# Kernel tuning notes

Measured on AMD Instinct MI355X. Metric: run time of the kernel, lower is better.

## Reference

```python
import jax, jax.numpy as jnp
import numpy as np

D_MODEL = 1024
D_HEAD = 64
N_HEADS = D_MODEL // D_HEAD
MAX_SEQ = 2048
BATCH = 2
SEQ = 2048


def setup_inputs() -> dict:
    key = jax.random.key(0)
    ks = jax.random.split(key, 10)
    s = 1.0 / np.sqrt(D_MODEL)
    return {
        "x": jax.random.normal(ks[0], (BATCH, SEQ, D_MODEL), dtype=jnp.float32),
        "Wq": jax.random.normal(ks[1], (D_MODEL, D_MODEL), dtype=jnp.float32) * s,
        "bq": jax.random.normal(ks[2], (D_MODEL,), dtype=jnp.float32) * 0.01,
        "Wk": jax.random.normal(ks[3], (D_MODEL, D_MODEL), dtype=jnp.float32) * s,
        "bk": jax.random.normal(ks[4], (D_MODEL,), dtype=jnp.float32) * 0.01,
        "Wv": jax.random.normal(ks[5], (D_MODEL, D_MODEL), dtype=jnp.float32) * s,
        "bv": jax.random.normal(ks[6], (D_MODEL,), dtype=jnp.float32) * 0.01,
        "Er": jax.random.normal(ks[7], (MAX_SEQ, D_HEAD), dtype=jnp.float32),
        "Wo": jax.random.normal(ks[8], (D_MODEL, D_MODEL), dtype=jnp.float32) * s,
        "bo": jax.random.normal(ks[9], (D_MODEL,), dtype=jnp.float32) * 0.01,
    }


def _s_rel(q, Er):
    # q: [B,H,S,Dh]; use last S rows of Er (start = max_seq - seq)
    S = q.shape[2]
    Er_slice = Er[Er.shape[0] - S:, :]                  # [S, Dh]
    qE = jnp.einsum("bhsd,ld->bhsl", q, Er_slice)       # [B,H,S,S]
    padded = jnp.pad(qE, ((0, 0), (0, 0), (0, 0), (1, 0)))  # [B,H,S,S+1]
    B, H, S1, S2 = padded.shape
    padded = padded.reshape(B, H, S2, S1)               # skew trick
    return padded[:, :, 1:, :]                          # [B,H,S,S]


def reference(x, Wq, bq, Wk, bk, Wv, bv, Er, Wo, bo):
    B, S, _ = x.shape
    scale = 1.0 / np.sqrt(D_HEAD)
    # projections (torch Linear: x @ W.T + b)
    def proj(W, b):
        return (x @ W.T + b).reshape(B, S, N_HEADS, D_HEAD).transpose(0, 2, 1, 3)
    q = proj(Wq, bq)   # [B,H,S,Dh]
    k = proj(Wk, bk)
    v = proj(Wv, bv)
    qk = jnp.einsum("bhsd,bhtd->bhst", q, k)            # [B,H,S,S]
    logits = (qk + _s_rel(q, Er)) * scale
    causal = jnp.tril(jnp.ones((S, S), dtype=bool))
    masked = jnp.where(causal[None, None], logits, -1e9)
    attn = jax.nn.softmax(masked, axis=-1)
    out = jnp.einsum("bhst,bhtd->bhsd", attn, v)        # [B,H,S,Dh]
    out = out.transpose(0, 2, 1, 3).reshape(B, S, D_MODEL)
    return out @ Wo.T + bo
```

## Files before the change

kernel.cpp:

```cpp
#include <hip/hip_runtime.h>
#include <hip/hip_bf16.h>

typedef short v8s __attribute__((ext_vector_type(8)));
typedef float v4f __attribute__((ext_vector_type(4)));
typedef __hip_bfloat16 bf16;

#define MFMA(a, b, c) __builtin_amdgcn_mfma_f32_16x16x32_bf16(a, b, c, 0, 0, 0)

__global__ __launch_bounds__(256) void cast_all(
    const float* __restrict__ x,  const float* __restrict__ wq,
    const float* __restrict__ wk, const float* __restrict__ wv,
    const float* __restrict__ wo, const float* __restrict__ er,
    bf16* __restrict__ xb,  bf16* __restrict__ wqb, bf16* __restrict__ wkb,
    bf16* __restrict__ wvb, bf16* __restrict__ wob, bf16* __restrict__ erb)
{
    const int r = blockIdx.y;
    const float* s; bf16* d; int n4;
    if      (r == 0) { s = x;  d = xb;  n4 = 1048576; }
    else if (r == 1) { s = wq; d = wqb; n4 = 262144;  }
    else if (r == 2) { s = wk; d = wkb; n4 = 262144;  }
    else if (r == 3) { s = wv; d = wvb; n4 = 262144;  }
    else if (r == 4) { s = wo; d = wob; n4 = 262144;  }
    else             { s = er; d = erb; n4 = 32768;   }
    const int i = blockIdx.x * 256 + threadIdx.x;
    if (i < n4) {
        const float4 v = ((const float4*)s)[i];
        bf16 t[4];
        t[0] = __float2bfloat16(v.x);
        t[1] = __float2bfloat16(v.y);
        t[2] = __float2bfloat16(v.z);
        t[3] = __float2bfloat16(v.w);
        ((uint2*)d)[i] = *(const uint2*)t;
    }
}

__global__ __launch_bounds__(256) void gemm_nt(
    const bf16* __restrict__ A,
    const bf16* __restrict__ W0, const bf16* __restrict__ W1, const bf16* __restrict__ W2,
    const float* __restrict__ b0, const float* __restrict__ b1, const float* __restrict__ b2,
    bf16* __restrict__ o0, bf16* __restrict__ o1, bf16* __restrict__ o2,
    float* __restrict__ outf, int headmajor)
{
    const int z = blockIdx.z;
    const bf16* W     = (z == 0) ? W0 : (z == 1) ? W1 : W2;
    const float* bias = (z == 0) ? b0 : (z == 1) ? b1 : b2;
    bf16* out         = (z == 0) ? o0 : (z == 1) ? o1 : o2;

    __shared__ bf16 As[128 * 40];
    __shared__ bf16 Bs[128 * 40];

    const int tid = threadIdx.x;
    const int w  = tid >> 6, l = tid & 63;
    const int lm = l & 15,  lq = l >> 4;
    const int wm = (w >> 1) * 64, wn = (w & 1) * 64;
    const int m0 = blockIdx.y * 128, n0 = blockIdx.x * 128;

    v4f acc[4][4];
#pragma unroll
    for (int i = 0; i < 4; ++i)
#pragma unroll
        for (int j = 0; j < 4; ++j) acc[i][j] = (v4f){0.f, 0.f, 0.f, 0.f};

    const int r0 = tid >> 2;
    const int c8 = (tid & 3) * 8;

    for (int k0 = 0; k0 < 1024; k0 += 32) {
        __syncthreads();
#pragma unroll
        for (int rep = 0; rep < 2; ++rep) {
            const int row = r0 + rep * 64;
            *(uint4*)&As[row * 40 + c8] = *(const uint4*)&A[(size_t)(m0 + row) * 1024 + k0 + c8];
            *(uint4*)&Bs[row * 40 + c8] = *(const uint4*)&W[(size_t)(n0 + row) * 1024 + k0 + c8];
        }
        __syncthreads();
        v8s a[4], b[4];
#pragma unroll
        for (int i = 0; i < 4; ++i) a[i] = *(const v8s*)&As[(wm + i * 16 + lm) * 40 + lq * 8];
#pragma unroll
        for (int j = 0; j < 4; ++j) b[j] = *(const v8s*)&Bs[(wn + j * 16 + lm) * 40 + lq * 8];
#pragma unroll
        for (int i = 0; i < 4; ++i)
#pragma unroll
            for (int j = 0; j < 4; ++j)
                acc[i][j] = MFMA(a[i], b[j], acc[i][j]);
    }

    float bv[4];
#pragma unroll
    for (int j = 0; j < 4; ++j) bv[j] = bias[n0 + wn + j * 16 + lm];

#pragma unroll
    for (int i = 0; i < 4; ++i) {
#pragma unroll
        for (int j = 0; j < 4; ++j) {
            const int col = n0 + wn + j * 16 + lm;
#pragma unroll
            for (int r = 0; r < 4; ++r) {
                const int row = m0 + wm + i * 16 + lq * 4 + r;
                const float v = acc[i][j][r] + bv[j];
                if (headmajor) {
                    const int bb = row >> 11, ss = row & 2047;
                    const int hh = col >> 6,  dd = col & 63;
                    out[((size_t)(bb * 16 + hh) * 2048 + ss) * 64 + dd] = __float2bfloat16(v);
                } else {
                    outf[(size_t)row * 1024 + col] = v;
                }
            }
        }
    }
}

__global__ __launch_bounds__(256) void vtrans(const bf16* __restrict__ V, bf16* __restrict__ Vt)
{
    __shared__ bf16 T[64 * 72];
    const int s0  = blockIdx.x * 64;
    const int bh  = blockIdx.y;
    const int tid = threadIdx.x;
#pragma unroll
    for (int rep = 0; rep < 2; ++rep) {
        const int unit = tid + rep * 256;
        const int sl = unit >> 3, d8 = (unit & 7) * 8;
        *(uint4*)&T[sl * 72 + d8] = *(const uint4*)&V[((size_t)bh * 2048 + s0 + sl) * 64 + d8];
    }
    __syncthreads();
#pragma unroll
    for (int rep = 0; rep < 2; ++rep) {
        const int unit = tid + rep * 256;
        const int d = unit >> 3, t8 = (unit & 7) * 8;
        unsigned short tmp[8];
#pragma unroll
        for (int j = 0; j < 8; ++j) tmp[j] = *(const unsigned short*)&T[(t8 + j) * 72 + d];
        *(uint4*)&Vt[((size_t)bh * 64 + d) * 2048 + s0 + t8] = *(const uint4*)tmp;
    }
}

__global__ __launch_bounds__(256, 4) void attn(
    const bf16* __restrict__ Q, const bf16* __restrict__ K,
    const bf16* __restrict__ Vt, const bf16* __restrict__ Er,
    bf16* __restrict__ AO)
{
    __shared__ bf16 Ks[64 * 72];
    __shared__ bf16 Vs[64 * 72];
    __shared__ bf16 Ps[64 * 72];
    __shared__ bf16 Gs[64 * 84];

    const int ord = blockIdx.x;
    const int u = ord & 255, j = ord >> 8;
    const int a = u & 31, yh = u >> 5;
    const int q1 = (j & 2) ? (a ^ 16) : a;
    const int qb = (j & 1) ? (31 - q1) : q1;
    const int bh = 8 * j + yh;

    const int i0 = qb * 64;
    const int b  = bh >> 4, h = bh & 15;
    const int tid = threadIdx.x;
    const int w  = tid >> 6, l = tid & 63;
    const int lm = l & 15,  lq = l >> 4;

    const bf16* qp = Q + ((size_t)bh * 2048 + i0 + w * 16 + lm) * 64 + lq * 8;
    const v8s q0 = *(const v8s*)qp;
    const v8s q1f = *(const v8s*)(qp + 32);

    v4f accO[4];
#pragma unroll
    for (int dt = 0; dt < 4; ++dt) accO[dt] = (v4f){0.f, 0.f, 0.f, 0.f};
    float rs[4];
#pragma unroll
    for (int r = 0; r < 4; ++r) rs[r] = 0.f;

    const int sr0 = tid >> 3;
    const int sc8 = (tid & 7) * 8;
    const size_t kbase = (size_t)bh * 2048 * 64;
    const size_t vbase = (size_t)bh * 64 * 2048;

    const int nk = qb + 1;

    uint4 kp0 = *(const uint4*)&K[kbase + (size_t)sr0 * 64 + sc8];
    uint4 kp1 = *(const uint4*)&K[kbase + (size_t)(sr0 + 32) * 64 + sc8];
    uint4 vp0 = *(const uint4*)&Vt[vbase + (size_t)sr0 * 2048 + sc8];
    uint4 vp1 = *(const uint4*)&Vt[vbase + (size_t)(sr0 + 32) * 2048 + sc8];

    for (int it = 0; it < nk; ++it) {
        const int j0 = it * 64;
        __syncthreads();
        *(uint4*)&Ks[sr0 * 72 + sc8]        = kp0;
        *(uint4*)&Ks[(sr0 + 32) * 72 + sc8] = kp1;
        *(uint4*)&Vs[sr0 * 72 + sc8]        = vp0;
        *(uint4*)&Vs[(sr0 + 32) * 72 + sc8] = vp1;
        if (it + 1 < nk) {
            const int jn = j0 + 64;
            kp0 = *(const uint4*)&K[kbase + (size_t)(jn + sr0) * 64 + sc8];
            kp1 = *(const uint4*)&K[kbase + (size_t)(jn + sr0 + 32) * 64 + sc8];
            vp0 = *(const uint4*)&Vt[vbase + (size_t)sr0 * 2048 + jn + sc8];
            vp1 = *(const uint4*)&Vt[vbase + (size_t)(sr0 + 32) * 2048 + jn + sc8];
        }
        const int basew = 2048 - 16 - i0 + j0 - 16 * w;
#pragma unroll
        for (int ct2 = 0; ct2 < 5; ++ct2) {
            int mr = basew + ct2 * 16 + lm;
            mr = (mr > 2047) ? 2047 : mr;
            const bf16* ep = Er + (size_t)mr * 64 + lq * 8;
            const v8s e0 = *(const v8s*)ep;
            const v8s e1 = *(const v8s*)(ep + 32);
            v4f g = (v4f){0.f, 0.f, 0.f, 0.f};
            g = MFMA(q0, e0, g);
            g = MFMA(q1f, e1, g);
#pragma unroll
            for (int r = 0; r < 4; ++r)
                Gs[(w * 16 + lq * 4 + r) * 84 + ct2 * 16 + lm] =
                    __float2bfloat16(g[r] * 0.125f);
        }
        __syncthreads();
        v4f sv[4];
#pragma unroll
        for (int ct = 0; ct < 4; ++ct) {
            const v8s k0f = *(const v8s*)&Ks[(ct * 16 + lm) * 72 + lq * 8];
            const v8s k1f = *(const v8s*)&Ks[(ct * 16 + lm) * 72 + 32 + lq * 8];
            v4f s = (v4f){0.f, 0.f, 0.f, 0.f};
            s = MFMA(q0, k0f, s);
            s = MFMA(q1f, k1f, s);
            sv[ct] = s;
        }
#pragma unroll
        for (int r = 0; r < 4; ++r) {
            const int rl = lq * 4 + r;
            const int ig = i0 + w * 16 + rl;
#pragma unroll
            for (int ct = 0; ct < 4; ++ct) {
                const int jj = ct * 16 + lm;
                const float gb = (float)Gs[(w * 16 + rl) * 84 + jj + 15 - rl];
                float s = fmaf(sv[ct][r], 0.125f, gb);
                if (j0 + jj > ig) s = -1e9f;
                const float pe = __expf(s - 4.0f);
                rs[r] += pe;
                Ps[(w * 16 + rl) * 72 + jj] = __float2bfloat16(pe);
            }
        }
        const v8s pa0 = *(const v8s*)&Ps[(w * 16 + lm) * 72 + lq * 8];
        const v8s pa1 = *(const v8s*)&Ps[(w * 16 + lm) * 72 + 32 + lq * 8];
#pragma unroll
        for (int dt = 0; dt < 4; ++dt) {
            const v8s vb0 = *(const v8s*)&Vs[(dt * 16 + lm) * 72 + lq * 8];
            const v8s vb1 = *(const v8s*)&Vs[(dt * 16 + lm) * 72 + 32 + lq * 8];
            accO[dt] = MFMA(pa0, vb0, accO[dt]);
            accO[dt] = MFMA(pa1, vb1, accO[dt]);
        }
    }
#pragma unroll
    for (int r = 0; r < 4; ++r) {
#pragma unroll
        for (int msk = 8; msk >= 1; msk >>= 1)
            rs[r] += __shfl_xor(rs[r], msk, 64);
    }
#pragma unroll
    for (int dt = 0; dt < 4; ++dt) {
#pragma unroll
        for (int r = 0; r < 4; ++r) {
            const int row = i0 + w * 16 + lq * 4 + r;
            const int d   = dt * 16 + lm;
            const float v = accO[dt][r] / rs[r];
            AO[((size_t)b * 2048 + row) * 1024 + h * 64 + d] = __float2bfloat16(v);
        }
    }
}

extern "C" void kernel_launch(void* const* d_in, const int* in_sizes, int n_in,
                              void* d_out, int out_size, void* d_ws, size_t ws_size,
                              hipStream_t stream)
{
    const float* x  = (const float*)d_in[0];
    const float* Wq = (const float*)d_in[1];
    const float* bq = (const float*)d_in[2];
    const float* Wk = (const float*)d_in[3];
    const float* bk = (const float*)d_in[4];
    const float* Wv = (const float*)d_in[5];
    const float* bv = (const float*)d_in[6];
    const float* Er = (const float*)d_in[7];
    const float* Wo = (const float*)d_in[8];
    const float* bo = (const float*)d_in[9];
    float* out = (float*)d_out;

    bf16* ws = (bf16*)d_ws;
    const size_t NEl = (size_t)4096 * 1024;
    bf16* Qw  = ws;
    bf16* Kw  = ws + NEl;
    bf16* Vw  = ws + 2 * NEl;
    bf16* Vtw = ws + 3 * NEl;
    bf16* xb  = ws + 4 * NEl;
    bf16* AOw = xb;
    bf16* Wqb = ws + 5 * NEl;
    bf16* Wkb = Wqb + 1024 * 1024;
    bf16* Wvb = Wkb + 1024 * 1024;
    bf16* Wob = Wvb + 1024 * 1024;
    bf16* Erb = Wob + 1024 * 1024;

    cast_all<<<dim3(4096, 6), 256, 0, stream>>>(x, Wq, Wk, Wv, Wo, Er,
                                                xb, Wqb, Wkb, Wvb, Wob, Erb);
    gemm_nt<<<dim3(8, 32, 3), 256, 0, stream>>>(xb, Wqb, Wkb, Wvb, bq, bk, bv,
                                                Qw, Kw, Vw, nullptr, 1);
    vtrans<<<dim3(32, 32), 256, 0, stream>>>(Vw, Vtw);
    attn<<<dim3(1024), 256, 0, stream>>>(Qw, Kw, Vtw, Erb, AOw);
    gemm_nt<<<dim3(8, 32, 1), 256, 0, stream>>>(AOw, Wob, Wob, Wob, bo, bo, bo,
                                                AOw, AOw, AOw, out, 0);
}
```

Measured before the change: 280.4 us.

## Split causal attention KV range across blocks with atomic partial sums

Attention work for long query blocks is split into up to four KV segments (2560 blocks instead of 1024). Each segment atomically adds its unnormalized output and row-sum into fp32 num/den buffers. The output projection GEMM normalizes and casts these on load, and the QKV GEMM casts x from fp32 on load, so the separate x cast disappears. This balances per-block work and raises parallelism, at the cost of a memset, fp32 atomics, and a larger fp32 intermediate read by the final GEMM. The fixed exp(s-4) shift with no running max is unchanged, so combining partial sums stays exact.

After: 297.4 us. 6.0% more time.

```diff
diff --git a/kernel.cpp b/kernel.cpp
--- a/kernel.cpp
+++ b/kernel.cpp
@@ -7,21 +7,20 @@
 
 #define MFMA(a, b, c) __builtin_amdgcn_mfma_f32_16x16x32_bf16(a, b, c, 0, 0, 0)
 
-__global__ __launch_bounds__(256) void cast_all(
-    const float* __restrict__ x,  const float* __restrict__ wq,
-    const float* __restrict__ wk, const float* __restrict__ wv,
-    const float* __restrict__ wo, const float* __restrict__ er,
-    bf16* __restrict__ xb,  bf16* __restrict__ wqb, bf16* __restrict__ wkb,
-    bf16* __restrict__ wvb, bf16* __restrict__ wob, bf16* __restrict__ erb)
+__global__ __launch_bounds__(256) void cast_w(
+    const float* __restrict__ wq, const float* __restrict__ wk,
+    const float* __restrict__ wv, const float* __restrict__ wo,
+    const float* __restrict__ er,
+    bf16* __restrict__ wqb, bf16* __restrict__ wkb, bf16* __restrict__ wvb,
+    bf16* __restrict__ wob, bf16* __restrict__ erb)
 {
     const int r = blockIdx.y;
     const float* s; bf16* d; int n4;
-    if      (r == 0) { s = x;  d = xb;  n4 = 1048576; }
-    else if (r == 1) { s = wq; d = wqb; n4 = 262144;  }
-    else if (r == 2) { s = wk; d = wkb; n4 = 262144;  }
-    else if (r == 3) { s = wv; d = wvb; n4 = 262144;  }
-    else if (r == 4) { s = wo; d = wob; n4 = 262144;  }
-    else             { s = er; d = erb; n4 = 32768;   }
+    if      (r == 0) { s = wq; d = wqb; n4 = 262144; }
+    else if (r == 1) { s = wk; d = wkb; n4 = 262144; }
+    else if (r == 2) { s = wv; d = wvb; n4 = 262144; }
+    else if (r == 3) { s = wo; d = wob; n4 = 262144; }
+    else             { s = er; d = erb; n4 = 32768;  }
     const int i = blockIdx.x * 256 + threadIdx.x;
     if (i < n4) {
         const float4 v = ((const float4*)s)[i];
@@ -34,12 +33,14 @@
     }
 }
 
+template<int MODE>
 __global__ __launch_bounds__(256) void gemm_nt(
-    const bf16* __restrict__ A,
+    const float* __restrict__ Af,
+    const float* __restrict__ num, const float* __restrict__ den,
     const bf16* __restrict__ W0, const bf16* __restrict__ W1, const bf16* __restrict__ W2,
     const float* __restrict__ b0, const float* __restrict__ b1, const float* __restrict__ b2,
     bf16* __restrict__ o0, bf16* __restrict__ o1, bf16* __restrict__ o2,
-    float* __restrict__ outf, int headmajor)
+    float* __restrict__ outf)
 {
     const int z = blockIdx.z;
     const bf16* W     = (z == 0) ? W0 : (z == 1) ? W1 : W2;
@@ -69,7 +70,29 @@
 #pragma unroll
         for (int rep = 0; rep < 2; ++rep) {
             const int row = r0 + rep * 64;
-            *(uint4*)&As[row * 40 + c8] = *(const uint4*)&A[(size_t)(m0 + row) * 1024 + k0 + c8];
+            bf16 t[8];
+            if (MODE == 0) {
+                const float4 f0 = *(const float4*)&Af[(size_t)(m0 + row) * 1024 + k0 + c8];
+                const float4 f1 = *(const float4*)&Af[(size_t)(m0 + row) * 1024 + k0 + c8 + 4];
+                t[0] = __float2bfloat16(f0.x); t[1] = __float2bfloat16(f0.y);
+                t[2] = __float2bfloat16(f0.z); t[3] = __float2bfloat16(f0.w);
+                t[4] = __float2bfloat16(f1.x); t[5] = __float2bfloat16(f1.y);
+                t[6] = __float2bfloat16(f1.z); t[7] = __float2bfloat16(f1.w);
+            } else {
+                const int rowg = m0 + row;
+                const int bb = rowg >> 11, ss = rowg & 2047;
+                const int col0 = k0 + c8;
+                const int hh = col0 >> 6, dd = col0 & 63;
+                const size_t rbase = ((size_t)(bb * 16 + hh) * 2048 + ss);
+                const float4 f0 = *(const float4*)&num[rbase * 64 + dd];
+                const float4 f1 = *(const float4*)&num[rbase * 64 + dd + 4];
+                const float rdn = 1.0f / den[rbase];
+                t[0] = __float2bfloat16(f0.x * rdn); t[1] = __float2bfloat16(f0.y * rdn);
+                t[2] = __float2bfloat16(f0.z * rdn); t[3] = __float2bfloat16(f0.w * rdn);
+                t[4] = __float2bfloat16(f1.x * rdn); t[5] = __float2bfloat16(f1.y * rdn);
+                t[6] = __float2bfloat16(f1.z * rdn); t[7] = __float2bfloat16(f1.w * rdn);
+            }
+            *(uint4*)&As[row * 40 + c8] = *(const uint4*)t;
             *(uint4*)&Bs[row * 40 + c8] = *(const uint4*)&W[(size_t)(n0 + row) * 1024 + k0 + c8];
         }
         __syncthreads();
@@ -98,7 +121,7 @@
             for (int r = 0; r < 4; ++r) {
                 const int row = m0 + wm + i * 16 + lq * 4 + r;
                 const float v = acc[i][j][r] + bv[j];
-                if (headmajor) {
+                if (MODE == 0) {
                     const int bb = row >> 11, ss = row & 2047;
                     const int hh = col >> 6,  dd = col & 63;
                     out[((size_t)(bb * 16 + hh) * 2048 + ss) * 64 + dd] = __float2bfloat16(v);
@@ -137,7 +160,7 @@
 __global__ __launch_bounds__(256, 4) void attn(
     const bf16* __restrict__ Q, const bf16* __restrict__ K,
     const bf16* __restrict__ Vt, const bf16* __restrict__ Er,
-    bf16* __restrict__ AO)
+    float* __restrict__ num, float* __restrict__ den)
 {
     __shared__ bf16 Ks[64 * 72];
     __shared__ bf16 Vs[64 * 72];
@@ -145,14 +168,18 @@
     __shared__ bf16 Gs[64 * 84];
 
     const int ord = blockIdx.x;
-    const int u = ord & 255, j = ord >> 8;
-    const int a = u & 31, yh = u >> 5;
-    const int q1 = (j & 2) ? (a ^ 16) : a;
-    const int qb = (j & 1) ? (31 - q1) : q1;
-    const int bh = 8 * j + yh;
+    const int bh  = ord / 80;
+    const int c   = 79 - (ord - bh * 80);
+    int qb, sp, ns;
+    if      (c < 8)  { qb = c;                  sp = 0;            ns = 1; }
+    else if (c < 24) { qb = 8  + ((c - 8) >> 1);  sp = (c - 8) & 1;  ns = 2; }
+    else if (c < 48) { qb = 16 + (c - 24) / 3;    sp = (c - 24) % 3; ns = 3; }
+    else             { qb = 24 + ((c - 48) >> 2); sp = (c - 48) & 3; ns = 4; }
+    const int n  = qb + 1;
+    const int t0 = (sp * n) / ns;
+    const int t1 = ((sp + 1) * n) / ns;
 
     const int i0 = qb * 64;
-    const int b  = bh >> 4, h = bh & 15;
     const int tid = threadIdx.x;
     const int w  = tid >> 6, l = tid & 63;
     const int lm = l & 15,  lq = l >> 4;
@@ -173,77 +200,78 @@
     const size_t kbase = (size_t)bh * 2048 * 64;
     const size_t vbase = (size_t)bh * 64 * 2048;
 
-    const int nk = qb + 1;
-
-    uint4 kp0 = *(const uint4*)&K[kbase + (size_t)sr0 * 64 + sc8];
-    uint4 kp1 = *(const uint4*)&K[kbase + (size_t)(sr0 + 32) * 64 + sc8];
-    uint4 vp0 = *(const uint4*)&Vt[vbase + (size_t)sr0 * 2048 + sc8];
-    uint4 vp1 = *(const uint4*)&Vt[vbase + (size_t)(sr0 + 32) * 2048 + sc8];
-
-    for (int it = 0; it < nk; ++it) {
-        const int j0 = it * 64;
-        __syncthreads();
-        *(uint4*)&Ks[sr0 * 72 + sc8]        = kp0;
-        *(uint4*)&Ks[(sr0 + 32) * 72 + sc8] = kp1;
-        *(uint4*)&Vs[sr0 * 72 + sc8]        = vp0;
-        *(uint4*)&Vs[(sr0 + 32) * 72 + sc8] = vp1;
-        if (it + 1 < nk) {
-            const int jn = j0 + 64;
-            kp0 = *(const uint4*)&K[kbase + (size_t)(jn + sr0) * 64 + sc8];
-            kp1 = *(const uint4*)&K[kbase + (size_t)(jn + sr0 + 32) * 64 + sc8];
-            vp0 = *(const uint4*)&Vt[vbase + (size_t)sr0 * 2048 + jn + sc8];
-            vp1 = *(const uint4*)&Vt[vbase + (size_t)(sr0 + 32) * 2048 + jn + sc8];
-        }
-        const int basew = 2048 - 16 - i0 + j0 - 16 * w;
-#pragma unroll
-        for (int ct2 = 0; ct2 < 5; ++ct2) {
-            int mr = basew + ct2 * 16 + lm;
-            mr = (mr > 2047) ? 2047 : mr;
-            const bf16* ep = Er + (size_t)mr * 64 + lq * 8;
-            const v8s e0 = *(const v8s*)ep;
-            const v8s e1 = *(const v8s*)(ep + 32);
-            v4f g = (v4f){0.f, 0.f, 0.f, 0.f};
-            g = MFMA(q0, e0, g);
-            g = MFMA(q1f, e1, g);
-#pragma unroll
-            for (int r = 0; r < 4; ++r)
-                Gs[(w * 16 + lq * 4 + r) * 84 + ct2 * 16 + lm] =
-                    __float2bfloat16(g[r] * 0.125f);
-        }
-        __syncthreads();
-        v4f sv[4];
-#pragma unroll
-        for (int ct = 0; ct < 4; ++ct) {
-            const v8s k0f = *(const v8s*)&Ks[(ct * 16 + lm) * 72 + lq * 8];
-            const v8s k1f = *(const v8s*)&Ks[(ct * 16 + lm) * 72 + 32 + lq * 8];
-            v4f s = (v4f){0.f, 0.f, 0.f, 0.f};
-            s = MFMA(q0, k0f, s);
-            s = MFMA(q1f, k1f, s);
-            sv[ct] = s;
-        }
-#pragma unroll
-        for (int r = 0; r < 4; ++r) {
-            const int rl = lq * 4 + r;
-            const int ig = i0 + w * 16 + rl;
+    {
+        const int j0 = t0 * 64;
+        uint4 kp0 = *(const uint4*)&K[kbase + (size_t)(j0 + sr0) * 64 + sc8];
+        uint4 kp1 = *(const uint4*)&K[kbase + (size_t)(j0 + sr0 + 32) * 64 + sc8];
+        uint4 vp0 = *(const uint4*)&Vt[vbase + (size_t)sr0 * 2048 + j0 + sc8];
+        uint4 vp1 = *(const uint4*)&Vt[vbase + (size_t)(sr0 + 32) * 2048 + j0 + sc8];
+
+        for (int it = t0; it < t1; ++it) {
+            const int j0i = it * 64;
+            __syncthreads();
+            *(uint4*)&Ks[sr0 * 72 + sc8]        = kp0;
+            *(uint4*)&Ks[(sr0 + 32) * 72 + sc8] = kp1;
+            *(uint4*)&Vs[sr0 * 72 + sc8]        = vp0;
+            *(uint4*)&Vs[(sr0 + 32) * 72 + sc8] = vp1;
+            if (it + 1 < t1) {
+                const int jn = j0i + 64;
+                kp0 = *(const uint4*)&K[kbase + (size_t)(jn + sr0) * 64 + sc8];
+                kp1 = *(const uint4*)&K[kbase + (size_t)(jn + sr0 + 32) * 64 + sc8];
+                vp0 = *(const uint4*)&Vt[vbase + (size_t)sr0 * 2048 + jn + sc8];
+                vp1 = *(const uint4*)&Vt[vbase + (size_t)(sr0 + 32) * 2048 + jn + sc8];
+            }
+            const int basew = 2048 - 16 - i0 + j0i - 16 * w;
+#pragma unroll
+            for (int ct2 = 0; ct2 < 5; ++ct2) {
+                int mr = basew + ct2 * 16 + lm;
+                mr = (mr > 2047) ? 2047 : mr;
+                const bf16* ep = Er + (size_t)mr * 64 + lq * 8;
+                const v8s e0 = *(const v8s*)ep;
+                const v8s e1 = *(const v8s*)(ep + 32);
+                v4f g = (v4f){0.f, 0.f, 0.f, 0.f};
+                g = MFMA(q0, e0, g);
+                g = MFMA(q1f, e1, g);
+#pragma unroll
+                for (int r = 0; r < 4; ++r)
+                    Gs[(w * 16 + lq * 4 + r) * 84 + ct2 * 16 + lm] =
+                        __float2bfloat16(g[r] * 0.125f);
+            }
+            __syncthreads();
+            v4f sv[4];
 #pragma unroll
             for (int ct = 0; ct < 4; ++ct) {
-                const int jj = ct * 16 + lm;
-                const float gb = (float)Gs[(w * 16 + rl) * 84 + jj + 15 - rl];
-                float s = fmaf(sv[ct][r], 0.125f, gb);
-                if (j0 + jj > ig) s = -1e9f;
-                const float pe = __expf(s - 4.0f);
-                rs[r] += pe;
-                Ps[(w * 16 + rl) * 72 + jj] = __float2bfloat16(pe);
-            }
-        }
-        const v8s pa0 = *(const v8s*)&Ps[(w * 16 + lm) * 72 + lq * 8];
-        const v8s pa1 = *(const v8s*)&Ps[(w * 16 + lm) * 72 + 32 + lq * 8];
-#pragma unroll
-        for (int dt = 0; dt < 4; ++dt) {
-            const v8s vb0 = *(const v8s*)&Vs[(dt * 16 + lm) * 72 + lq * 8];
-            const v8s vb1 = *(const v8s*)&Vs[(dt * 16 + lm) * 72 + 32 + lq * 8];
-            accO[dt] = MFMA(pa0, vb0, accO[dt]);
-            accO[dt] = MFMA(pa1, vb1, accO[dt]);
+                const v8s k0f = *(const v8s*)&Ks[(ct * 16 + lm) * 72 + lq * 8];
+                const v8s k1f = *(const v8s*)&Ks[(ct * 16 + lm) * 72 + 32 + lq * 8];
+                v4f s = (v4f){0.f, 0.f, 0.f, 0.f};
+                s = MFMA(q0, k0f, s);
+                s = MFMA(q1f, k1f, s);
+                sv[ct] = s;
+            }
+#pragma unroll
+            for (int r = 0; r < 4; ++r) {
+                const int rl = lq * 4 + r;
+                const int ig = i0 + w * 16 + rl;
+#pragma unroll
+                for (int ct = 0; ct < 4; ++ct) {
+                    const int jj = ct * 16 + lm;
+                    const float gb = (float)Gs[(w * 16 + rl) * 84 + jj + 15 - rl];
+                    float s = fmaf(sv[ct][r], 0.125f, gb);
+                    if (j0i + jj > ig) s = -1e9f;
+                    const float pe = __expf(s - 4.0f);
+                    rs[r] += pe;
+                    Ps[(w * 16 + rl) * 72 + jj] = __float2bfloat16(pe);
+                }
+            }
+            const v8s pa0 = *(const v8s*)&Ps[(w * 16 + lm) * 72 + lq * 8];
+            const v8s pa1 = *(const v8s*)&Ps[(w * 16 + lm) * 72 + 32 + lq * 8];
+#pragma unroll
+            for (int dt = 0; dt < 4; ++dt) {
+                const v8s vb0 = *(const v8s*)&Vs[(dt * 16 + lm) * 72 + lq * 8];
+                const v8s vb1 = *(const v8s*)&Vs[(dt * 16 + lm) * 72 + 32 + lq * 8];
+                accO[dt] = MFMA(pa0, vb0, accO[dt]);
+                accO[dt] = MFMA(pa1, vb1, accO[dt]);
+            }
         }
     }
 #pragma unroll
@@ -252,15 +280,18 @@
         for (int msk = 8; msk >= 1; msk >>= 1)
             rs[r] += __shfl_xor(rs[r], msk, 64);
     }
+    const int rowb = i0 + w * 16 + lq * 4;
 #pragma unroll
     for (int dt = 0; dt < 4; ++dt) {
 #pragma unroll
-        for (int r = 0; r < 4; ++r) {
-            const int row = i0 + w * 16 + lq * 4 + r;
-            const int d   = dt * 16 + lm;
-            const float v = accO[dt][r] / rs[r];
-            AO[((size_t)b * 2048 + row) * 1024 + h * 64 + d] = __float2bfloat16(v);
-        }
+        for (int r = 0; r < 4; ++r)
+            atomicAdd(&num[((size_t)bh * 2048 + rowb + r) * 64 + dt * 16 + lm],
+                      accO[dt][r]);
+    }
+    if (lm == 0) {
+#pragma unroll
+        for (int r = 0; r < 4; ++r)
+            atomicAdd(&den[(size_t)bh * 2048 + rowb + r], rs[r]);
     }
 }
 
@@ -280,26 +311,29 @@
     const float* bo = (const float*)d_in[9];
     float* out = (float*)d_out;
 
-    bf16* ws = (bf16*)d_ws;
+    char* wsb = (char*)d_ws;
+    float* num = (float*)wsb;
+    float* den = (float*)(wsb + 16777216);
+    bf16* wsh = (bf16*)(wsb + 17039360);
     const size_t NEl = (size_t)4096 * 1024;
-    bf16* Qw  = ws;
-    bf16* Kw  = ws + NEl;
-    bf16* Vw  = ws + 2 * NEl;
-    bf16* Vtw = ws + 3 * NEl;
-    bf16* xb  = ws + 4 * NEl;
-    bf16* AOw = xb;
-    bf16* Wqb = ws + 5 * NEl;
-    bf16* Wkb = Wqb + 1024 * 1024;
-    bf16* Wvb = Wkb + 1024 * 1024;
-    bf16* Wob = Wvb + 1024 * 1024;
-    bf16* Erb = Wob + 1024 * 1024;
-
-    cast_all<<<dim3(4096, 6), 256, 0, stream>>>(x, Wq, Wk, Wv, Wo, Er,
-                                                xb, Wqb, Wkb, Wvb, Wob, Erb);
-    gemm_nt<<<dim3(8, 32, 3), 256, 0, stream>>>(xb, Wqb, Wkb, Wvb, bq, bk, bv,
-                                                Qw, Kw, Vw, nullptr, 1);
+    bf16* Qw  = wsh;
+    bf16* Kw  = Qw + NEl;
+    bf16* Vw  = Kw + NEl;
+    bf16* Vtw = Vw + NEl;
+    bf16* Wqb = Vtw + NEl;
+    bf16* Wkb = Wqb + 1048576;
+    bf16* Wvb = Wkb + 1048576;
+    bf16* Wob = Wvb + 1048576;
+    bf16* Erb = Wob + 1048576;
+
+    hipMemsetAsync(num, 0, 17039360, stream);
+    cast_w<<<dim3(1024, 5), 256, 0, stream>>>(Wq, Wk, Wv, Wo, Er,
+                                              Wqb, Wkb, Wvb, Wob, Erb);
+    gemm_nt<0><<<dim3(8, 32, 3), 256, 0, stream>>>(
+        x, nullptr, nullptr, Wqb, Wkb, Wvb, bq, bk, bv, Qw, Kw, Vw, nullptr);
     vtrans<<<dim3(32, 32), 256, 0, stream>>>(Vw, Vtw);
-    attn<<<dim3(1024), 256, 0, stream>>>(Qw, Kw, Vtw, Erb, AOw);
-    gemm_nt<<<dim3(8, 32, 1), 256, 0, stream>>>(AOw, Wob, Wob, Wob, bo, bo, bo,
-                                                AOw, AOw, AOw, out, 0);
-}
+    attn<<<dim3(2560), 256, 0, stream>>>(Qw, Kw, Vtw, Erb, num, den);
+    gemm_nt<1><<<dim3(8, 32, 1), 256, 0, stream>>>(
+        nullptr, num, den, Wob, Wob, Wob, bo, bo, bo,
+        nullptr, nullptr, nullptr, out);
+}
```
